# Performance work log

Measured on AMD Instinct MI355X. Metric: run time of the kernel, lower is better.

The kernel has to match this reference:

```python
import jax, jax.numpy as jnp
import numpy as np

B, L, H = 1024, 256, 128
NUM_TEAMS, NUM_VENUES, NUM_RESULTS = 1000, 3, 3
OUT_IN = 4 * H + 2 + 3  # past_repr (4H+2) concat stats (3)


def setup_inputs() -> dict:
    key = jax.random.key(0)
    ks = jax.random.split(key, 16)
    return {
        "team_embed": jax.random.normal(ks[0], (NUM_TEAMS, H), jnp.float32) * 0.02,
        "venue_embed": jax.random.normal(ks[1], (NUM_VENUES, H), jnp.float32) * 0.02,
        "result_embed": jax.random.normal(ks[2], (NUM_RESULTS, H), jnp.float32) * 0.02,
        "W_out": jax.random.normal(ks[3], (OUT_IN, NUM_RESULTS), jnp.float32) * 0.02,
        "b_out": jnp.zeros((NUM_RESULTS,), jnp.float32),
        "goals_for": jax.random.uniform(ks[4], (B, L), jnp.float32) * 5.0,
        "goals_against": jax.random.uniform(ks[5], (B, L), jnp.float32) * 5.0,
        "stats": jax.random.uniform(ks[6], (B, 3), jnp.float32),
        "venue": jax.random.randint(ks[7], (B, L), 0, NUM_VENUES),
        "team": jax.random.randint(ks[8], (B, L), 0, NUM_TEAMS),
        "opponent": jax.random.randint(ks[9], (B, L), 0, NUM_TEAMS),
        "result": jax.random.randint(ks[10], (B, L), 0, NUM_RESULTS),
        "next_venue": jax.random.randint(ks[11], (B,), 0, NUM_VENUES),
        "next_team": jax.random.randint(ks[12], (B,), 0, NUM_TEAMS),
        "next_opponent": jax.random.randint(ks[13], (B,), 0, NUM_TEAMS),
    }


def reference(team_embed, venue_embed, result_embed, W_out, b_out,
              goals_for, goals_against, stats,
              venue, team, opponent, result,
              next_venue, next_team, next_opponent):
    h = team_embed.shape[1]
    # (B, L, 4H+2): embedding gathers + goal scalars concatenated
    past_seq = jnp.concatenate([
        venue_embed[venue], team_embed[team], team_embed[opponent],
        result_embed[result], goals_for[..., None], goals_against[..., None],
    ], axis=-1)
    # (B, 3H): next-match condition vector
    next_cond = jnp.concatenate([
        venue_embed[next_venue], team_embed[next_team], team_embed[next_opponent],
    ], axis=-1)
    scale = jnp.asarray(3 * h, past_seq.dtype) ** 0.5
    scores = jnp.einsum('bld,bd->bl', past_seq[..., : 3 * h], next_cond) / scale
    attn = jax.nn.softmax(scores, axis=1)                 # over L
    past_repr = jnp.einsum('bl,bld->bd', attn, past_seq)  # (B, 4H+2)
    logits = jnp.concatenate([past_repr, stats], axis=-1) @ W_out + b_out
    return logits
```

## Files before the change

kernel.cpp:

```cpp
#include <hip/hip_runtime.h>

#define L_ 256
#define H_ 128

#define KSCALE 0.07362222315f

template <int CTRL>
__device__ __forceinline__ float dpp_add(float v) {
    return v + __int_as_float(__builtin_amdgcn_update_dpp(
        0, __float_as_int(v), CTRL, 0xF, 0xF, true));
}

__device__ __forceinline__ float dppReduce16(float v) {
    v = dpp_add<0xB1>(v);
    v = dpp_add<0x4E>(v);
    v = dpp_add<0x141>(v);
    v = dpp_add<0x140>(v);
    return v;
}

__device__ __forceinline__ float dppReduce64(float v) {
    v = dppReduce16(v);
    v = dpp_add<0x142>(v);
    v = dpp_add<0x143>(v);
    return v;
}

__global__ __launch_bounds__(256) void fused_match_kernel(
    const float* __restrict__ team_embed,
    const float* __restrict__ venue_embed,
    const float* __restrict__ result_embed,
    const float* __restrict__ W_out,
    const float* __restrict__ b_out,
    const float* __restrict__ goals_for,
    const float* __restrict__ goals_against,
    const float* __restrict__ stats,
    const int* __restrict__ venue,
    const int* __restrict__ team,
    const int* __restrict__ opponent,
    const int* __restrict__ result,
    const int* __restrict__ next_venue,
    const int* __restrict__ next_team,
    const int* __restrict__ next_opponent,
    float* __restrict__ out)
{
    const int b    = blockIdx.x;
    const int t    = threadIdx.x;
    const int lane = t & 63;
    const int wid  = t >> 6;
    const int grp  = lane >> 4;
    const int ci   = lane & 15;

    __shared__ float  nc[384];
    __shared__ int    s_team[L_];
    __shared__ int    s_opp[L_];
    __shared__ float  s_score[L_];
    __shared__ float  s_dv[L_];
    __shared__ float  s_dotv[3];
    __shared__ float  s_m[16];
    __shared__ float4 s_accT[16][32];
    __shared__ float4 s_accO[16][32];
    __shared__ float  s_reds[4];
    __shared__ float  s_redw[4][8];
    __shared__ float  s_w[8];
    __shared__ float  s_pr[517];

    const int base = b * L_;
    const int my_venue  = venue[base + t];
    const int my_result = result[base + t];
    const float my_gf   = goals_for[base + t];
    const float my_ga   = goals_against[base + t];
    s_team[t] = team[base + t];
    s_opp[t]  = opponent[base + t];

    const int nv  = next_venue[b];
    const int ntm = next_team[b];
    const int nop = next_opponent[b];
    if (t < 128) {
        nc[t]       = venue_embed[nv * H_ + t];
        nc[128 + t] = team_embed[ntm * H_ + t];
    } else {
        nc[128 + t] = team_embed[nop * H_ + (t - 128)];
    }
    __syncthreads();

    if (wid < 3) {
        float a = venue_embed[wid * H_ + lane]      * nc[lane]
                + venue_embed[wid * H_ + 64 + lane] * nc[64 + lane];
        a = dppReduce64(a);
        if (lane == 63) s_dotv[wid] = a;
    }
    __syncthreads();
    s_dv[t] = s_dotv[my_venue];
    __syncthreads();

    const float4 nct0 = ((const float4*)(nc + 128))[ci];
    const float4 nct1 = ((const float4*)(nc + 128))[ci + 16];
    const float4 nco0 = ((const float4*)(nc + 256))[ci];
    const float4 nco1 = ((const float4*)(nc + 256))[ci + 16];

    const int lb = wid * 64;
    float4 accT0 = make_float4(0.f, 0.f, 0.f, 0.f);
    float4 accT1 = make_float4(0.f, 0.f, 0.f, 0.f);
    float4 accO0 = make_float4(0.f, 0.f, 0.f, 0.f);
    float4 accO1 = make_float4(0.f, 0.f, 0.f, 0.f);
    float  mrun = -1e30f;
    #pragma unroll 2
    for (int i = 0; i < 16; ++i) {
        const int l = lb + i * 4 + grp;
        const float4* rT = (const float4*)team_embed + s_team[l] * 32;
        const float4* rO = (const float4*)team_embed + s_opp[l]  * 32;
        const float4 vT0 = rT[ci];
        const float4 vT1 = rT[ci + 16];
        const float4 vO0 = rO[ci];
        const float4 vO1 = rO[ci + 16];
        float p = vT0.x * nct0.x + vT0.y * nct0.y + vT0.z * nct0.z + vT0.w * nct0.w
                + vT1.x * nct1.x + vT1.y * nct1.y + vT1.z * nct1.z + vT1.w * nct1.w
                + vO0.x * nco0.x + vO0.y * nco0.y + vO0.z * nco0.z + vO0.w * nco0.w
                + vO1.x * nco1.x + vO1.y * nco1.y + vO1.z * nco1.z + vO1.w * nco1.w;
        p = dppReduce16(p);
        const float kk = (p + s_dv[l]) * KSCALE;
        if (ci == 0) s_score[l] = kk;
        if (kk > mrun) {
            const float alpha = exp2f(mrun - kk);
            accT0.x *= alpha; accT0.y *= alpha; accT0.z *= alpha; accT0.w *= alpha;
            accT1.x *= alpha; accT1.y *= alpha; accT1.z *= alpha; accT1.w *= alpha;
            accO0.x *= alpha; accO0.y *= alpha; accO0.z *= alpha; accO0.w *= alpha;
            accO1.x *= alpha; accO1.y *= alpha; accO1.z *= alpha; accO1.w *= alpha;
            mrun = kk;
        }
        const float e = exp2f(kk - mrun);
        accT0.x += e * vT0.x; accT0.y += e * vT0.y; accT0.z += e * vT0.z; accT0.w += e * vT0.w;
        accT1.x += e * vT1.x; accT1.y += e * vT1.y; accT1.z += e * vT1.z; accT1.w += e * vT1.w;
        accO0.x += e * vO0.x; accO0.y += e * vO0.y; accO0.z += e * vO0.z; accO0.w += e * vO0.w;
        accO1.x += e * vO1.x; accO1.y += e * vO1.y; accO1.z += e * vO1.z; accO1.w += e * vO1.w;
    }
    {
        const int hs = wid * 4 + grp;
        if (ci == 0) s_m[hs] = mrun;
        s_accT[hs][ci]      = accT0;
        s_accT[hs][ci + 16] = accT1;
        s_accO[hs][ci]      = accO0;
        s_accO[hs][ci + 16] = accO1;
    }
    __syncthreads();

    float M = s_m[0];
    #pragma unroll
    for (int j = 1; j < 16; ++j) M = fmaxf(M, s_m[j]);

    const float e = exp2f(s_score[t] - M);
    float vals[8];
    vals[0] = (my_venue  == 0) ? e : 0.f;
    vals[1] = (my_venue  == 1) ? e : 0.f;
    vals[2] = (my_venue  == 2) ? e : 0.f;
    vals[3] = (my_result == 0) ? e : 0.f;
    vals[4] = (my_result == 1) ? e : 0.f;
    vals[5] = (my_result == 2) ? e : 0.f;
    vals[6] = e * my_gf;
    vals[7] = e * my_ga;
    float sum = dppReduce64(e);
    #pragma unroll
    for (int k = 0; k < 8; ++k) vals[k] = dppReduce64(vals[k]);
    if (lane == 63) {
        s_reds[wid] = sum;
        #pragma unroll
        for (int k = 0; k < 8; ++k) s_redw[wid][k] = vals[k];
    }
    __syncthreads();
    const float Z    = s_reds[0] + s_reds[1] + s_reds[2] + s_reds[3];
    const float invZ = 1.f / Z;
    if (t < 8)
        s_w[t] = (s_redw[0][t] + s_redw[1][t] + s_redw[2][t] + s_redw[3][t]) * invZ;
    __syncthreads();

    if (t < 64) {
        const int seg = t >> 5;
        const int cc  = t & 31;
        float4 a = make_float4(0.f, 0.f, 0.f, 0.f);
        #pragma unroll
        for (int h = 0; h < 16; ++h) {
            const float sc  = exp2f(s_m[h] - M);
            const float4 v  = seg ? s_accO[h][cc] : s_accT[h][cc];
            a.x += sc * v.x; a.y += sc * v.y; a.z += sc * v.z; a.w += sc * v.w;
        }
        const int d = 128 + seg * 128 + cc * 4;
        s_pr[d + 0] = a.x * invZ;
        s_pr[d + 1] = a.y * invZ;
        s_pr[d + 2] = a.z * invZ;
        s_pr[d + 3] = a.w * invZ;
        if (t < 2) s_pr[512 + t] = s_w[6 + t];
        if (t >= 2 && t < 5) s_pr[512 + t] = stats[b * 3 + t - 2];
    } else if (t < 192) {
        const int j = t - 64;
        s_pr[j] = s_w[0] * venue_embed[j] + s_w[1] * venue_embed[H_ + j]
                + s_w[2] * venue_embed[2 * H_ + j];
    } else {
        const int j = t - 192;
        s_pr[384 + j] = s_w[3] * result_embed[j]      + s_w[4] * result_embed[H_ + j]
                      + s_w[5] * result_embed[2 * H_ + j];
        s_pr[448 + j] = s_w[3] * result_embed[64 + j] + s_w[4] * result_embed[H_ + 64 + j]
                      + s_w[5] * result_embed[2 * H_ + 64 + j];
    }
    __syncthreads();

    if (wid < 3) {
        float acc = 0.f;
        for (int d = lane; d < 517; d += 64) acc += s_pr[d] * W_out[d * 3 + wid];
        acc = dppReduce64(acc);
        if (lane == 63) out[b * 3 + wid] = acc + b_out[wid];
    }
}

extern "C" void kernel_launch(void* const* d_in, const int* in_sizes, int n_in,
                              void* d_out, int out_size, void* d_ws, size_t ws_size,
                              hipStream_t stream) {
    const float* team_embed    = (const float*)d_in[0];
    const float* venue_embed   = (const float*)d_in[1];
    const float* result_embed  = (const float*)d_in[2];
    const float* W_out         = (const float*)d_in[3];
    const float* b_out         = (const float*)d_in[4];
    const float* goals_for     = (const float*)d_in[5];
    const float* goals_against = (const float*)d_in[6];
    const float* stats         = (const float*)d_in[7];
    const int* venue           = (const int*)d_in[8];
    const int* team            = (const int*)d_in[9];
    const int* opponent        = (const int*)d_in[10];
    const int* result          = (const int*)d_in[11];
    const int* next_venue      = (const int*)d_in[12];
    const int* next_team       = (const int*)d_in[13];
    const int* next_opponent   = (const int*)d_in[14];
    float* out = (float*)d_out;

    const int B = in_sizes[12];
    fused_match_kernel<<<B, 256, 0, stream>>>(
        team_embed, venue_embed, result_embed, W_out, b_out,
        goals_for, goals_against, stats,
        venue, team, opponent, result,
        next_venue, next_team, next_opponent, out);
}
```

Baseline: 101.9 us.

## Drop softmax max tracking, prefetch next gather rows, and trim reductions and barriers

Removes the online-softmax running max and rescaling. Scores are exponentiated directly and the stored exp values feed the final reductions, which cuts the max pass, the per-head rescaling and one barrier. The team/opponent embedding gathers are software-prefetched one iteration ahead to hide global-load latency. The per-block venue dot product is now looked up on the fly instead of going through an extra shared array and barrier. The reduction count drops from nine to seven by deriving the last venue and result weights as one minus the others. The cost is that softmax without max subtraction can overflow for large scores, and the sum-to-one trick adds some rounding error.

Result: slower. 104.6 us (+2.7%).

```diff
diff --git a/kernel.cpp b/kernel.cpp
--- a/kernel.cpp
+++ b/kernel.cpp
@@ -54,15 +54,12 @@
     __shared__ float  nc[384];
     __shared__ int    s_team[L_];
     __shared__ int    s_opp[L_];
-    __shared__ float  s_score[L_];
-    __shared__ float  s_dv[L_];
+    __shared__ int    s_venue[L_];
+    __shared__ float  s_e[L_];
     __shared__ float  s_dotv[3];
-    __shared__ float  s_m[16];
     __shared__ float4 s_accT[16][32];
     __shared__ float4 s_accO[16][32];
-    __shared__ float  s_reds[4];
-    __shared__ float  s_redw[4][8];
-    __shared__ float  s_w[8];
+    __shared__ float  s_redw[4][7];
     __shared__ float  s_pr[517];
 
     const int base = b * L_;
@@ -70,8 +67,9 @@
     const int my_result = result[base + t];
     const float my_gf   = goals_for[base + t];
     const float my_ga   = goals_against[base + t];
-    s_team[t] = team[base + t];
-    s_opp[t]  = opponent[base + t];
+    s_team[t]  = team[base + t];
+    s_opp[t]   = opponent[base + t];
+    s_venue[t] = my_venue;
 
     const int nv  = next_venue[b];
     const int ntm = next_team[b];
@@ -91,53 +89,61 @@
         if (lane == 63) s_dotv[wid] = a;
     }
     __syncthreads();
-    s_dv[t] = s_dotv[my_venue];
-    __syncthreads();
 
     const float4 nct0 = ((const float4*)(nc + 128))[ci];
     const float4 nct1 = ((const float4*)(nc + 128))[ci + 16];
     const float4 nco0 = ((const float4*)(nc + 256))[ci];
     const float4 nco1 = ((const float4*)(nc + 256))[ci + 16];
 
+    const float4* te4 = (const float4*)team_embed;
     const int lb = wid * 64;
+
     float4 accT0 = make_float4(0.f, 0.f, 0.f, 0.f);
     float4 accT1 = make_float4(0.f, 0.f, 0.f, 0.f);
     float4 accO0 = make_float4(0.f, 0.f, 0.f, 0.f);
     float4 accO1 = make_float4(0.f, 0.f, 0.f, 0.f);
-    float  mrun = -1e30f;
-    #pragma unroll 2
-    for (int i = 0; i < 16; ++i) {
-        const int l = lb + i * 4 + grp;
-        const float4* rT = (const float4*)team_embed + s_team[l] * 32;
-        const float4* rO = (const float4*)team_embed + s_opp[l]  * 32;
-        const float4 vT0 = rT[ci];
-        const float4 vT1 = rT[ci + 16];
-        const float4 vO0 = rO[ci];
-        const float4 vO1 = rO[ci + 16];
-        float p = vT0.x * nct0.x + vT0.y * nct0.y + vT0.z * nct0.z + vT0.w * nct0.w
-                + vT1.x * nct1.x + vT1.y * nct1.y + vT1.z * nct1.z + vT1.w * nct1.w
-                + vO0.x * nco0.x + vO0.y * nco0.y + vO0.z * nco0.z + vO0.w * nco0.w
-                + vO1.x * nco1.x + vO1.y * nco1.y + vO1.z * nco1.z + vO1.w * nco1.w;
-        p = dppReduce16(p);
-        const float kk = (p + s_dv[l]) * KSCALE;
-        if (ci == 0) s_score[l] = kk;
-        if (kk > mrun) {
-            const float alpha = exp2f(mrun - kk);
-            accT0.x *= alpha; accT0.y *= alpha; accT0.z *= alpha; accT0.w *= alpha;
-            accT1.x *= alpha; accT1.y *= alpha; accT1.z *= alpha; accT1.w *= alpha;
-            accO0.x *= alpha; accO0.y *= alpha; accO0.z *= alpha; accO0.w *= alpha;
-            accO1.x *= alpha; accO1.y *= alpha; accO1.z *= alpha; accO1.w *= alpha;
-            mrun = kk;
+
+    {
+        const int l0 = lb + grp;
+        const int iT = s_team[l0] * 32;
+        const int iO = s_opp[l0]  * 32;
+        float4 vT0 = te4[iT + ci];
+        float4 vT1 = te4[iT + 16 + ci];
+        float4 vO0 = te4[iO + ci];
+        float4 vO1 = te4[iO + 16 + ci];
+        float  dv  = s_dotv[s_venue[l0]];
+
+        #pragma unroll 4
+        for (int i = 0; i < 16; ++i) {
+            const float4 cT0 = vT0, cT1 = vT1, cO0 = vO0, cO1 = vO1;
+            const float  cdv = dv;
+            const int    cl  = lb + i * 4 + grp;
+            if (i < 15) {
+                const int ln = cl + 4;
+                const int jT = s_team[ln] * 32;
+                const int jO = s_opp[ln]  * 32;
+                vT0 = te4[jT + ci];
+                vT1 = te4[jT + 16 + ci];
+                vO0 = te4[jO + ci];
+                vO1 = te4[jO + 16 + ci];
+                dv  = s_dotv[s_venue[ln]];
+            }
+            float p0 = cT0.x * nct0.x + cT0.y * nct0.y + cT0.z * nct0.z + cT0.w * nct0.w;
+            float p1 = cT1.x * nct1.x + cT1.y * nct1.y + cT1.z * nct1.z + cT1.w * nct1.w;
+            float p2 = cO0.x * nco0.x + cO0.y * nco0.y + cO0.z * nco0.z + cO0.w * nco0.w;
+            float p3 = cO1.x * nco1.x + cO1.y * nco1.y + cO1.z * nco1.z + cO1.w * nco1.w;
+            float p  = (p0 + p1) + (p2 + p3);
+            p = dppReduce16(p);
+            const float e = exp2f((p + cdv) * KSCALE);
+            if (ci == 0) s_e[cl] = e;
+            accT0.x += e * cT0.x; accT0.y += e * cT0.y; accT0.z += e * cT0.z; accT0.w += e * cT0.w;
+            accT1.x += e * cT1.x; accT1.y += e * cT1.y; accT1.z += e * cT1.z; accT1.w += e * cT1.w;
+            accO0.x += e * cO0.x; accO0.y += e * cO0.y; accO0.z += e * cO0.z; accO0.w += e * cO0.w;
+            accO1.x += e * cO1.x; accO1.y += e * cO1.y; accO1.z += e * cO1.z; accO1.w += e * cO1.w;
         }
-        const float e = exp2f(kk - mrun);
-        accT0.x += e * vT0.x; accT0.y += e * vT0.y; accT0.z += e * vT0.z; accT0.w += e * vT0.w;
-        accT1.x += e * vT1.x; accT1.y += e * vT1.y; accT1.z += e * vT1.z; accT1.w += e * vT1.w;
-        accO0.x += e * vO0.x; accO0.y += e * vO0.y; accO0.z += e * vO0.z; accO0.w += e * vO0.w;
-        accO1.x += e * vO1.x; accO1.y += e * vO1.y; accO1.z += e * vO1.z; accO1.w += e * vO1.w;
     }
     {
         const int hs = wid * 4 + grp;
-        if (ci == 0) s_m[hs] = mrun;
         s_accT[hs][ci]      = accT0;
         s_accT[hs][ci + 16] = accT1;
         s_accO[hs][ci]      = accO0;
@@ -145,34 +151,26 @@
     }
     __syncthreads();
 
-    float M = s_m[0];
-    #pragma unroll
-    for (int j = 1; j < 16; ++j) M = fmaxf(M, s_m[j]);
-
-    const float e = exp2f(s_score[t] - M);
-    float vals[8];
-    vals[0] = (my_venue  == 0) ? e : 0.f;
-    vals[1] = (my_venue  == 1) ? e : 0.f;
-    vals[2] = (my_venue  == 2) ? e : 0.f;
-    vals[3] = (my_result == 0) ? e : 0.f;
-    vals[4] = (my_result == 1) ? e : 0.f;
-    vals[5] = (my_result == 2) ? e : 0.f;
-    vals[6] = e * my_gf;
-    vals[7] = e * my_ga;
-    float sum = dppReduce64(e);
-    #pragma unroll
-    for (int k = 0; k < 8; ++k) vals[k] = dppReduce64(vals[k]);
-    if (lane == 63) {
-        s_reds[wid] = sum;
+    {
+        const float e = s_e[t];
+        float vals[7];
+        vals[0] = e;
+        vals[1] = (my_venue  == 0) ? e : 0.f;
+        vals[2] = (my_venue  == 1) ? e : 0.f;
+        vals[3] = (my_result == 0) ? e : 0.f;
+        vals[4] = (my_result == 1) ? e : 0.f;
+        vals[5] = e * my_gf;
+        vals[6] = e * my_ga;
         #pragma unroll
-        for (int k = 0; k < 8; ++k) s_redw[wid][k] = vals[k];
-    }
-    __syncthreads();
-    const float Z    = s_reds[0] + s_reds[1] + s_reds[2] + s_reds[3];
-    const float invZ = 1.f / Z;
-    if (t < 8)
-        s_w[t] = (s_redw[0][t] + s_redw[1][t] + s_redw[2][t] + s_redw[3][t]) * invZ;
-    __syncthreads();
+        for (int k = 0; k < 7; ++k) vals[k] = dppReduce64(vals[k]);
+        if (lane == 63) {
+            #pragma unroll
+            for (int k = 0; k < 7; ++k) s_redw[wid][k] = vals[k];
+        }
+    }
+    __syncthreads();
+
+    #define RW(k) (s_redw[0][k] + s_redw[1][k] + s_redw[2][k] + s_redw[3][k])
 
     if (t < 64) {
         const int seg = t >> 5;
@@ -180,28 +178,37 @@
         float4 a = make_float4(0.f, 0.f, 0.f, 0.f);
         #pragma unroll
         for (int h = 0; h < 16; ++h) {
-            const float sc  = exp2f(s_m[h] - M);
-            const float4 v  = seg ? s_accO[h][cc] : s_accT[h][cc];
-            a.x += sc * v.x; a.y += sc * v.y; a.z += sc * v.z; a.w += sc * v.w;
+            const float4 v = seg ? s_accO[h][cc] : s_accT[h][cc];
+            a.x += v.x; a.y += v.y; a.z += v.z; a.w += v.w;
         }
+        const float invZ = 1.f / RW(0);
         const int d = 128 + seg * 128 + cc * 4;
         s_pr[d + 0] = a.x * invZ;
         s_pr[d + 1] = a.y * invZ;
         s_pr[d + 2] = a.z * invZ;
         s_pr[d + 3] = a.w * invZ;
-        if (t < 2) s_pr[512 + t] = s_w[6 + t];
+        if (t < 2) s_pr[512 + t] = RW(5 + t) * invZ;
         if (t >= 2 && t < 5) s_pr[512 + t] = stats[b * 3 + t - 2];
     } else if (t < 192) {
         const int j = t - 64;
-        s_pr[j] = s_w[0] * venue_embed[j] + s_w[1] * venue_embed[H_ + j]
-                + s_w[2] * venue_embed[2 * H_ + j];
+        const float invZ = 1.f / RW(0);
+        const float w0 = RW(1) * invZ;
+        const float w1 = RW(2) * invZ;
+        const float w2 = 1.f - w0 - w1;
+        s_pr[j] = w0 * venue_embed[j] + w1 * venue_embed[H_ + j]
+                + w2 * venue_embed[2 * H_ + j];
     } else {
         const int j = t - 192;
-        s_pr[384 + j] = s_w[3] * result_embed[j]      + s_w[4] * result_embed[H_ + j]
-                      + s_w[5] * result_embed[2 * H_ + j];
-        s_pr[448 + j] = s_w[3] * result_embed[64 + j] + s_w[4] * result_embed[H_ + 64 + j]
-                      + s_w[5] * result_embed[2 * H_ + 64 + j];
-    }
+        const float invZ = 1.f / RW(0);
+        const float w3 = RW(3) * invZ;
+        const float w4 = RW(4) * invZ;
+        const float w5 = 1.f - w3 - w4;
+        s_pr[384 + j] = w3 * result_embed[j]      + w4 * result_embed[H_ + j]
+                      + w5 * result_embed[2 * H_ + j];
+        s_pr[448 + j] = w3 * result_embed[64 + j] + w4 * result_embed[H_ + 64 + j]
+                      + w5 * result_embed[2 * H_ + 64 + j];
+    }
+    #undef RW
     __syncthreads();
 
     if (wid < 3) {
```
